# Performance work log

Hardware: AMD Instinct MI355X
Metric: run time of the kernel (lower is better)

The kernel has to match this reference:

```python
import jax, jax.numpy as jnp
import numpy as np

N_HEAD = 16          # word_dim=1024 -> head_dim=64
SCALE = True         # scale_attentions=True
NEG_INF = -1.0e9


def setup_inputs() -> dict:
    key = jax.random.key(0)
    k0, k1, k2 = jax.random.split(key, 3)
    B, S, D = 8, 1024, 1024
    x = jax.random.normal(k0, (B, S, D), dtype=jnp.float32)
    W_qkv = jax.random.normal(k1, (D, 3 * D), dtype=jnp.float32) * 0.02
    b_qkv = jnp.zeros((3 * D,), dtype=jnp.float32)
    W_out = jax.random.normal(k2, (D, D), dtype=jnp.float32) * 0.02
    b_out = jnp.zeros((D,), dtype=jnp.float32)
    return {"x": x, "W_qkv": W_qkv, "b_qkv": b_qkv, "W_out": W_out, "b_out": b_out}


def reference(x, W_qkv, b_qkv, W_out, b_out):
    B, S, D = x.shape
    dh = D // N_HEAD
    # fused QKV pointwise (kernel_size=1 conv == linear) projection
    qkv = x @ W_qkv + b_qkv                      # [B, S, 3D]
    q, k, v = jnp.split(qkv, 3, axis=-1)         # each [B, S, D]

    def heads(t):
        return t.reshape(B, S, N_HEAD, dh).transpose(0, 2, 1, 3)  # [B, H, S, dh]

    q, k, v = heads(q), heads(k), heads(v)
    scores = jnp.einsum('bhqd,bhkd->bhqk', q, k)  # [B, H, S, S]
    if SCALE:
        scores = scores / jnp.sqrt(jnp.asarray(dh, scores.dtype))
    # custom causal masking: multiplicative mask + additive large-negative term
    mask = jnp.tril(jnp.ones((S, S), dtype=scores.dtype))  # [S, S]
    scores = scores * mask + NEG_INF * (1.0 - mask)
    w = jax.nn.softmax(scores, axis=-1)          # attn_dropout is identity in eval
    out = jnp.einsum('bhqk,bhkd->bhqd', w, v)    # [B, H, S, dh]
    out = out.transpose(0, 2, 1, 3).reshape(B, S, D)  # regroup heads
    return out @ W_out + b_out                   # output_dropout is identity in eval
```

## Files before the change

kernel.cpp:

```cpp
#include <hip/hip_runtime.h>
#include <hip/hip_bf16.h>

typedef __attribute__((ext_vector_type(8))) short short8;
typedef __attribute__((ext_vector_type(4))) float f32x4;
typedef __attribute__((ext_vector_type(4))) unsigned short us4;

#define GK 1024

__device__ __forceinline__ unsigned short f2bf(float f) {
  unsigned int u = __float_as_uint(f);
  u += 0x7fffu + ((u >> 16) & 1u);
  return (unsigned short)(u >> 16);
}

__device__ __forceinline__ void gload16(const void* g, void* lds_base ) {
  __builtin_amdgcn_global_load_lds(
      (const __attribute__((address_space(1))) unsigned int*)g,
      (__attribute__((address_space(3))) unsigned int*)lds_base, 16, 0, 0);
}

__global__ void cast4_f32_bf16(const float* __restrict__ in, unsigned short* __restrict__ out, int n) {
  int i = (blockIdx.x * 256 + threadIdx.x) * 4;
  if (i >= n) return;
  float4 v = *(const float4*)(in + i);
  us4 o = { f2bf(v.x), f2bf(v.y), f2bf(v.z), f2bf(v.w) };
  *(us4*)(out + i) = o;
}

__global__ void transcast(const float* __restrict__ in, unsigned short* __restrict__ out, int K, int N) {
  __shared__ float t[32][33];
  int n0 = blockIdx.x * 32, k0 = blockIdx.y * 32;
  int tx = threadIdx.x, ty = threadIdx.y;
#pragma unroll
  for (int i = 0; i < 4; ++i)
    t[ty * 4 + i][tx] = in[(size_t)(k0 + ty * 4 + i) * N + n0 + tx];
  __syncthreads();
#pragma unroll
  for (int i = 0; i < 4; ++i)
    out[(size_t)(n0 + ty * 4 + i) * K + k0 + tx] = f2bf(t[tx][ty * 4 + i]);
}

template <int OUT_BF16>
__global__ __launch_bounds__(256) void gemm_nt(
    const unsigned short* __restrict__ A,
    const unsigned short* __restrict__ Bt,
    const float* __restrict__ bias,
    void* __restrict__ C, int M, int N)
{
  __shared__ __align__(16) unsigned short Asm[128 * 32];
  __shared__ __align__(16) unsigned short Bsm[128 * 32];
  int bm = blockIdx.x, bn = blockIdx.y;
  int t = threadIdx.x, w = t >> 6, l = t & 63;
  int wm = w >> 1, wn = w & 1;
  int g = l >> 4, ln = l & 15;

  const unsigned short* Ablk = A + (size_t)(bm * 128) * GK;
  const unsigned short* Bblk = Bt + (size_t)(bn * 128) * GK;

  f32x4 acc[4][4] = {};

  int r0 = (w << 4) + (l >> 2);
  int kc = (l & 3) * 8;

  for (int kt = 0; kt < GK / 32; ++kt) {
    __syncthreads();
    int k0 = kt * 32 + kc;
    gload16(Ablk + (size_t)r0 * GK + k0,        Asm + w * 512);
    gload16(Ablk + (size_t)(r0 + 64) * GK + k0, Asm + (4 + w) * 512);
    gload16(Bblk + (size_t)r0 * GK + k0,        Bsm + w * 512);
    gload16(Bblk + (size_t)(r0 + 64) * GK + k0, Bsm + (4 + w) * 512);
    __syncthreads();

    short8 af[4], bf[4];
    int ar = wm * 64 + ln;
    int br = wn * 64 + ln;
    int kk = g * 8;
#pragma unroll
    for (int mt = 0; mt < 4; ++mt)
      af[mt] = *(const short8*)(Asm + (ar + mt * 16) * 32 + kk);
#pragma unroll
    for (int nt = 0; nt < 4; ++nt)
      bf[nt] = *(const short8*)(Bsm + (br + nt * 16) * 32 + kk);
#pragma unroll
    for (int mt = 0; mt < 4; ++mt)
#pragma unroll
      for (int nt = 0; nt < 4; ++nt)
        acc[mt][nt] = __builtin_amdgcn_mfma_f32_16x16x32_bf16(af[mt], bf[nt], acc[mt][nt], 0, 0, 0);
  }

  int rowb = bm * 128 + wm * 64 + (g << 2);
  int colb = bn * 128 + wn * 64 + ln;
#pragma unroll
  for (int nt = 0; nt < 4; ++nt) {
    int col = colb + nt * 16;
    float bv = bias[col];
#pragma unroll
    for (int mt = 0; mt < 4; ++mt) {
      int row = rowb + mt * 16;
#pragma unroll
      for (int r = 0; r < 4; ++r) {
        float v = acc[mt][nt][r] + bv;
        if (OUT_BF16) ((unsigned short*)C)[(size_t)(row + r) * N + col] = f2bf(v);
        else          ((float*)C)[(size_t)(row + r) * N + col] = v;
      }
    }
  }
}

__global__ void transpose_v(const unsigned short* __restrict__ qkvb, unsigned short* __restrict__ Vt) {
  __shared__ __align__(16) unsigned short tile[64][72];
  int blk = blockIdx.x;
  int st = blk & 15, bh = blk >> 4, h = bh & 15, b = bh >> 4;
  int t = threadIdx.x;
  int srow = t >> 2, c0 = (t & 3) * 2;

  const unsigned short* src = qkvb + (size_t)(b * 1024 + st * 64 + srow) * 3072 + 2048 + h * 64;
#pragma unroll
  for (int j = 0; j < 2; ++j)
    *(short8*)(&tile[srow][(c0 + j) * 8]) = *(const short8*)(src + (c0 + j) * 8);
  __syncthreads();

  int d = t >> 2;
  unsigned short* dst = Vt + (size_t)(bh * 64 + d) * 1024 + st * 64;
#pragma unroll
  for (int j = 0; j < 2; ++j) {
    int s0 = (c0 + j) * 8;
    short8 v;
#pragma unroll
    for (int i = 0; i < 8; ++i) v[i] = tile[s0 + i][d];
    *(short8*)(dst + s0) = v;
  }
}

__global__ __launch_bounds__(256) void attn(
    const unsigned short* __restrict__ qkv,
    const unsigned short* __restrict__ Vt,
    unsigned short* __restrict__ Ob)
{
  __shared__ __align__(16) unsigned short Ksm[2][64 * 64];
  __shared__ __align__(16) unsigned short Vsm[2][64 * 64];
  __shared__ __align__(16) unsigned short Psm[4][16 * 64];

  int t = threadIdx.x, w = t >> 6, l = t & 63;
  int g = l >> 4, ln = l & 15;
  int blk = blockIdx.x;
  int bh = blk & 127, pb = blk >> 7;
  int h = bh & 15, b = bh >> 4;

  const unsigned short* Kg = qkv + (size_t)(b * 1024) * 3072 + 1024 + h * 64;
  const unsigned short* Vg = Vt + (size_t)(bh * 64) * 1024;
  unsigned short* P = Psm[w];

  int jrow = l >> 3;
  int jc   = l & 7;

  int cur = 0;

  auto stage = [&](int buf, int kt) {
#pragma unroll
    for (int jj = 0; jj < 2; ++jj) {
      int j = 2 * w + jj;
      int row = j * 8 + jrow;
      int sc = jc ^ (row & 7);
      gload16(Kg + (size_t)(kt * 64 + row) * 3072 + sc * 8, (unsigned short*)Ksm[buf] + j * 512);
      gload16(Vg + (size_t)row * 1024 + kt * 64 + sc * 8,   (unsigned short*)Vsm[buf] + j * 512);
    }
  };

#pragma unroll
  for (int half = 0; half < 2; ++half) {
    int qt = half ? (15 - pb) : pb;

    const unsigned short* qbase =
        qkv + (size_t)(b * 1024 + qt * 64 + w * 16 + ln) * 3072 + h * 64 + g * 8;
    short8 qf0 = *(const short8*)(qbase);
    short8 qf1 = *(const short8*)(qbase + 32);

    f32x4 acc_o[4] = {};
    float m_r[4], l_r[4];
#pragma unroll
    for (int r = 0; r < 4; ++r) { m_r[r] = -1.0e30f; l_r[r] = 0.f; }

    stage(cur, 0);
    __syncthreads();

    for (int kt = 0; kt <= qt; ++kt) {
      bool last = (kt == qt);
      if (!last) stage(cur ^ 1, kt + 1);

      const unsigned short* Kb = Ksm[cur];
      f32x4 s[4] = {};
#pragma unroll
      for (int nt = 0; nt < 4; ++nt) {
        int krow = nt * 16 + ln;
        short8 b0 = *(const short8*)(Kb + krow * 64 + ((g ^ (krow & 7)) * 8));
        short8 b1 = *(const short8*)(Kb + krow * 64 + (((4 + g) ^ (krow & 7)) * 8));
        s[nt] = __builtin_amdgcn_mfma_f32_16x16x32_bf16(qf0, b0, s[nt], 0, 0, 0);
        s[nt] = __builtin_amdgcn_mfma_f32_16x16x32_bf16(qf1, b1, s[nt], 0, 0, 0);
      }

      if (last) {
        int qrow = w * 16 + g * 4;
#pragma unroll
        for (int nt = 0; nt < 4; ++nt)
#pragma unroll
          for (int r = 0; r < 4; ++r)
            if (nt * 16 + ln > qrow + r) s[nt][r] = -1.0e9f;
      }

#pragma unroll
      for (int r = 0; r < 4; ++r) {
        float mraw = fmaxf(fmaxf(s[0][r], s[1][r]), fmaxf(s[2][r], s[3][r]));
#pragma unroll
        for (int off = 8; off >= 1; off >>= 1) mraw = fmaxf(mraw, __shfl_xor(mraw, off));
        float mnew = fmaxf(m_r[r], mraw * 0.125f);
        float corr = __expf(m_r[r] - mnew);
        m_r[r] = mnew;
        float rs = 0.f;
#pragma unroll
        for (int nt = 0; nt < 4; ++nt) {
          float p = __expf(fmaf(s[nt][r], 0.125f, -mnew));
          s[nt][r] = p;
          rs += p;
        }
#pragma unroll
        for (int off = 8; off >= 1; off >>= 1) rs += __shfl_xor(rs, off);
        l_r[r] = fmaf(l_r[r], corr, rs);
#pragma unroll
        for (int nt = 0; nt < 4; ++nt) acc_o[nt][r] *= corr;
      }

#pragma unroll
      for (int nt = 0; nt < 4; ++nt) {
        int col = nt * 16 + ln;
#pragma unroll
        for (int r = 0; r < 4; ++r) {
          int prow = g * 4 + r;
          P[prow * 64 + (((col >> 3) ^ (prow & 7)) * 8) + (col & 7)] = f2bf(s[nt][r]);
        }
      }
      short8 pa0 = *(const short8*)(P + ln * 64 + ((g ^ (ln & 7)) * 8));
      short8 pa1 = *(const short8*)(P + ln * 64 + (((4 + g) ^ (ln & 7)) * 8));

      const unsigned short* Vb = Vsm[cur];
#pragma unroll
      for (int nt = 0; nt < 4; ++nt) {
        int vrow = nt * 16 + ln;
        short8 vb0 = *(const short8*)(Vb + vrow * 64 + ((g ^ (vrow & 7)) * 8));
        short8 vb1 = *(const short8*)(Vb + vrow * 64 + (((4 + g) ^ (vrow & 7)) * 8));
        acc_o[nt] = __builtin_amdgcn_mfma_f32_16x16x32_bf16(pa0, vb0, acc_o[nt], 0, 0, 0);
        acc_o[nt] = __builtin_amdgcn_mfma_f32_16x16x32_bf16(pa1, vb1, acc_o[nt], 0, 0, 0);
      }

      __syncthreads();
      cur ^= 1;
    }

    float inv[4];
#pragma unroll
    for (int r = 0; r < 4; ++r) inv[r] = 1.0f / l_r[r];
    int orow = b * 1024 + qt * 64 + w * 16;
#pragma unroll
    for (int nt = 0; nt < 4; ++nt) {
      int col = h * 64 + nt * 16 + ln;
#pragma unroll
      for (int r = 0; r < 4; ++r)
        Ob[(size_t)(orow + g * 4 + r) * 1024 + col] = f2bf(acc_o[nt][r] * inv[r]);
    }
  }
}

extern "C" void kernel_launch(void* const* d_in, const int* in_sizes, int n_in,
                              void* d_out, int out_size, void* d_ws, size_t ws_size,
                              hipStream_t stream) {
  (void)in_sizes; (void)n_in; (void)out_size; (void)ws_size;
  const float* x    = (const float*)d_in[0];
  const float* Wqkv = (const float*)d_in[1];
  const float* bqkv = (const float*)d_in[2];
  const float* Wout = (const float*)d_in[3];
  const float* bout = (const float*)d_in[4];

  char* ws = (char*)d_ws;
  unsigned short* xb   = (unsigned short*)(ws);
  unsigned short* Wt1  = (unsigned short*)(ws + 16777216);
  unsigned short* Wt2  = (unsigned short*)(ws + 23068672);
  unsigned short* qkvb = (unsigned short*)(ws + 25165824);
  unsigned short* Vt   = (unsigned short*)(ws + 75497472);
  unsigned short* Ob   = (unsigned short*)(ws + 92274688);

  cast4_f32_bf16<<<8192, 256, 0, stream>>>(x, xb, 8192 * 1024);
  transcast<<<dim3(96, 32), dim3(32, 8), 0, stream>>>(Wqkv, Wt1, 1024, 3072);
  transcast<<<dim3(32, 32), dim3(32, 8), 0, stream>>>(Wout, Wt2, 1024, 1024);

  gemm_nt<1><<<dim3(64, 24), 256, 0, stream>>>(xb, Wt1, bqkv, qkvb, 8192, 3072);
  transpose_v<<<2048, 256, 0, stream>>>(qkvb, Vt);
  attn<<<1024, 256, 0, stream>>>(qkvb, Vt, Ob);
  gemm_nt<0><<<dim3(64, 8), 256, 0, stream>>>(Ob, Wt2, bout, (float*)d_out, 8192, 1024);
}
```

Measured before the change: 265.7 us.

## Transpose attention MFMA layout, use exp2 softmax with lazy rescale, swizzle GEMM tiles

The attention MFMAs swap operands so each lane owns one query row. Row max and sum then need only two cross-lane shuffles instead of four per row, and P and O can be written as packed 4-element stores. Softmax uses exp2 with the scale folded into log2(e)/8, and the rescale of the running max and accumulator is skipped when no lane's max grew. The GEMM block index is remapped into stripes of 8 M-tiles for better L2 reuse.

```diff
diff --git a/kernel.cpp b/kernel.cpp
--- a/kernel.cpp
+++ b/kernel.cpp
@@ -6,6 +6,8 @@
 typedef __attribute__((ext_vector_type(4))) unsigned short us4;
 
 #define GK 1024
+
+#define EXP2F(x) __builtin_amdgcn_exp2f(x)
 
 __device__ __forceinline__ unsigned short f2bf(float f) {
   unsigned int u = __float_as_uint(f);
@@ -49,7 +51,14 @@
 {
   __shared__ __align__(16) unsigned short Asm[128 * 32];
   __shared__ __align__(16) unsigned short Bsm[128 * 32];
-  int bm = blockIdx.x, bn = blockIdx.y;
+
+  int flat = blockIdx.y * gridDim.x + blockIdx.x;
+  int span = 8 * gridDim.y;
+  int stripe = flat / span;
+  int r = flat - stripe * span;
+  int bm = stripe * 8 + (r & 7);
+  int bn = r >> 3;
+
   int t = threadIdx.x, w = t >> 6, l = t & 63;
   int wm = w >> 1, wn = w & 1;
   int g = l >> 4, ln = l & 15;
@@ -98,10 +107,10 @@
     for (int mt = 0; mt < 4; ++mt) {
       int row = rowb + mt * 16;
 #pragma unroll
-      for (int r = 0; r < 4; ++r) {
-        float v = acc[mt][nt][r] + bv;
-        if (OUT_BF16) ((unsigned short*)C)[(size_t)(row + r) * N + col] = f2bf(v);
-        else          ((float*)C)[(size_t)(row + r) * N + col] = v;
+      for (int r2 = 0; r2 < 4; ++r2) {
+        float v = acc[mt][nt][r2] + bv;
+        if (OUT_BF16) ((unsigned short*)C)[(size_t)(row + r2) * N + col] = f2bf(v);
+        else          ((float*)C)[(size_t)(row + r2) * N + col] = v;
       }
     }
   }
@@ -141,6 +150,8 @@
   __shared__ __align__(16) unsigned short Vsm[2][64 * 64];
   __shared__ __align__(16) unsigned short Psm[4][16 * 64];
 
+  const float C1 = 0.18033688011112042f;
+
   int t = threadIdx.x, w = t >> 6, l = t & 63;
   int g = l >> 4, ln = l & 15;
   int blk = blockIdx.x;
@@ -153,7 +164,6 @@
 
   int jrow = l >> 3;
   int jc   = l & 7;
-
   int cur = 0;
 
   auto stage = [&](int buf, int kt) {
@@ -167,6 +177,8 @@
     }
   };
 
+  int pwbase = ln * 64 + (g & 1) * 4;
+
 #pragma unroll
   for (int half = 0; half < 2; ++half) {
     int qt = half ? (15 - pb) : pb;
@@ -177,9 +189,7 @@
     short8 qf1 = *(const short8*)(qbase + 32);
 
     f32x4 acc_o[4] = {};
-    float m_r[4], l_r[4];
-#pragma unroll
-    for (int r = 0; r < 4; ++r) { m_r[r] = -1.0e30f; l_r[r] = 0.f; }
+    float m2 = -1.0e30f, lsum = 0.f;
 
     stage(cur, 0);
     __syncthreads();
@@ -193,51 +203,58 @@
 #pragma unroll
       for (int nt = 0; nt < 4; ++nt) {
         int krow = nt * 16 + ln;
-        short8 b0 = *(const short8*)(Kb + krow * 64 + ((g ^ (krow & 7)) * 8));
-        short8 b1 = *(const short8*)(Kb + krow * 64 + (((4 + g) ^ (krow & 7)) * 8));
-        s[nt] = __builtin_amdgcn_mfma_f32_16x16x32_bf16(qf0, b0, s[nt], 0, 0, 0);
-        s[nt] = __builtin_amdgcn_mfma_f32_16x16x32_bf16(qf1, b1, s[nt], 0, 0, 0);
+        short8 k0 = *(const short8*)(Kb + krow * 64 + ((g ^ (krow & 7)) * 8));
+        short8 k1 = *(const short8*)(Kb + krow * 64 + (((4 + g) ^ (krow & 7)) * 8));
+        s[nt] = __builtin_amdgcn_mfma_f32_16x16x32_bf16(k0, qf0, s[nt], 0, 0, 0);
+        s[nt] = __builtin_amdgcn_mfma_f32_16x16x32_bf16(k1, qf1, s[nt], 0, 0, 0);
       }
 
       if (last) {
-        int qrow = w * 16 + g * 4;
+        int qrow = w * 16 + ln;
 #pragma unroll
         for (int nt = 0; nt < 4; ++nt)
 #pragma unroll
           for (int r = 0; r < 4; ++r)
-            if (nt * 16 + ln > qrow + r) s[nt][r] = -1.0e9f;
-      }
-
-#pragma unroll
-      for (int r = 0; r < 4; ++r) {
-        float mraw = fmaxf(fmaxf(s[0][r], s[1][r]), fmaxf(s[2][r], s[3][r]));
-#pragma unroll
-        for (int off = 8; off >= 1; off >>= 1) mraw = fmaxf(mraw, __shfl_xor(mraw, off));
-        float mnew = fmaxf(m_r[r], mraw * 0.125f);
-        float corr = __expf(m_r[r] - mnew);
-        m_r[r] = mnew;
-        float rs = 0.f;
-#pragma unroll
-        for (int nt = 0; nt < 4; ++nt) {
-          float p = __expf(fmaf(s[nt][r], 0.125f, -mnew));
+            if (nt * 16 + g * 4 + r > qrow) s[nt][r] = -1.0e9f;
+      }
+
+      float mx0 = fmaxf(fmaxf(s[0][0], s[0][1]), fmaxf(s[0][2], s[0][3]));
+      float mx1 = fmaxf(fmaxf(s[1][0], s[1][1]), fmaxf(s[1][2], s[1][3]));
+      float mx2 = fmaxf(fmaxf(s[2][0], s[2][1]), fmaxf(s[2][2], s[2][3]));
+      float mx3 = fmaxf(fmaxf(s[3][0], s[3][1]), fmaxf(s[3][2], s[3][3]));
+      float mraw = fmaxf(fmaxf(mx0, mx1), fmaxf(mx2, mx3));
+      mraw = fmaxf(mraw, __shfl_xor(mraw, 16));
+      mraw = fmaxf(mraw, __shfl_xor(mraw, 32));
+      float m2cand = mraw * C1;
+
+      if (!__all(m2cand <= m2)) {
+        float m2new = fmaxf(m2, m2cand);
+        float corr = EXP2F(m2 - m2new);
+        m2 = m2new;
+        lsum *= corr;
+#pragma unroll
+        for (int nt = 0; nt < 4; ++nt)
+#pragma unroll
+          for (int r = 0; r < 4; ++r) acc_o[nt][r] *= corr;
+      }
+
+      float rs = 0.f;
+#pragma unroll
+      for (int nt = 0; nt < 4; ++nt)
+#pragma unroll
+        for (int r = 0; r < 4; ++r) {
+          float p = EXP2F(fmaf(s[nt][r], C1, -m2));
           s[nt][r] = p;
           rs += p;
         }
-#pragma unroll
-        for (int off = 8; off >= 1; off >>= 1) rs += __shfl_xor(rs, off);
-        l_r[r] = fmaf(l_r[r], corr, rs);
-#pragma unroll
-        for (int nt = 0; nt < 4; ++nt) acc_o[nt][r] *= corr;
-      }
+      rs += __shfl_xor(rs, 16);
+      rs += __shfl_xor(rs, 32);
+      lsum += rs;
 
 #pragma unroll
       for (int nt = 0; nt < 4; ++nt) {
-        int col = nt * 16 + ln;
-#pragma unroll
-        for (int r = 0; r < 4; ++r) {
-          int prow = g * 4 + r;
-          P[prow * 64 + (((col >> 3) ^ (prow & 7)) * 8) + (col & 7)] = f2bf(s[nt][r]);
-        }
+        us4 pk = { f2bf(s[nt][0]), f2bf(s[nt][1]), f2bf(s[nt][2]), f2bf(s[nt][3]) };
+        *(us4*)(P + pwbase + (((nt * 2 + (g >> 1)) ^ (ln & 7)) * 8)) = pk;
       }
       short8 pa0 = *(const short8*)(P + ln * 64 + ((g ^ (ln & 7)) * 8));
       short8 pa1 = *(const short8*)(P + ln * 64 + (((4 + g) ^ (ln & 7)) * 8));
@@ -248,24 +265,21 @@
         int vrow = nt * 16 + ln;
         short8 vb0 = *(const short8*)(Vb + vrow * 64 + ((g ^ (vrow & 7)) * 8));
         short8 vb1 = *(const short8*)(Vb + vrow * 64 + (((4 + g) ^ (vrow & 7)) * 8));
-        acc_o[nt] = __builtin_amdgcn_mfma_f32_16x16x32_bf16(pa0, vb0, acc_o[nt], 0, 0, 0);
-        acc_o[nt] = __builtin_amdgcn_mfma_f32_16x16x32_bf16(pa1, vb1, acc_o[nt], 0, 0, 0);
+        acc_o[nt] = __builtin_amdgcn_mfma_f32_16x16x32_bf16(vb0, pa0, acc_o[nt], 0, 0, 0);
+        acc_o[nt] = __builtin_amdgcn_mfma_f32_16x16x32_bf16(vb1, pa1, acc_o[nt], 0, 0, 0);
       }
 
       __syncthreads();
       cur ^= 1;
     }
 
-    float inv[4];
-#pragma unroll
-    for (int r = 0; r < 4; ++r) inv[r] = 1.0f / l_r[r];
-    int orow = b * 1024 + qt * 64 + w * 16;
+    float inv = 1.0f / lsum;
+    size_t orow = (size_t)(b * 1024 + qt * 64 + w * 16 + ln);
 #pragma unroll
     for (int nt = 0; nt < 4; ++nt) {
-      int col = h * 64 + nt * 16 + ln;
-#pragma unroll
-      for (int r = 0; r < 4; ++r)
-        Ob[(size_t)(orow + g * 4 + r) * 1024 + col] = f2bf(acc_o[nt][r] * inv[r]);
+      us4 o = { f2bf(acc_o[nt][0] * inv), f2bf(acc_o[nt][1] * inv),
+                f2bf(acc_o[nt][2] * inv), f2bf(acc_o[nt][3] * inv) };
+      *(us4*)(Ob + orow * 1024 + h * 64 + nt * 16 + g * 4) = o;
     }
   }
 }
```

Measured after the change: 243.3 us. 1.09x faster.
